# Kernel optimization log

Hardware: AMD Instinct MI355X
Metric: run time of the kernel (lower is better)

Reference implementation:

```python
import jax, jax.numpy as jnp
import numpy as np

D = 1024
H = 16
HD = D // H
DFF = 4 * D
LN_EPS = 1e-5

def layernorm(x, gamma, beta):
    mu = jnp.mean(x, axis=-1, keepdims=True)
    var = jnp.mean(jnp.square(x - mu), axis=-1, keepdims=True)
    return (x - mu) * jax.lax.rsqrt(var + LN_EPS) * gamma + beta

def setup_inputs() -> dict:
    key = jax.random.key(0)
    ks = jax.random.split(key, 10)
    B, Nq, Nk = 2, 2048, 2048
    s = 0.02
    return {
        "q_x": jax.random.normal(ks[0], (B, Nq, D), jnp.float32),
        "kv_x": jax.random.normal(ks[1], (B, Nk, D), jnp.float32),
        "Wq": jax.random.normal(ks[2], (D, D), jnp.float32) * s,
        "Wkv": jax.random.normal(ks[3], (2 * D, D), jnp.float32) * s,
        "Wo": jax.random.normal(ks[4], (D, D), jnp.float32) * s,
        "bo": jnp.zeros((D,), jnp.float32),
        "ln_q_g": jnp.ones((D,), jnp.float32),
        "ln_q_b": jnp.zeros((D,), jnp.float32),
        "ln_kv_g": jnp.ones((D,), jnp.float32),
        "ln_kv_b": jnp.zeros((D,), jnp.float32),
        "W1": jax.random.normal(ks[5], (DFF, D), jnp.float32) * s,
        "b1": jnp.zeros((DFF,), jnp.float32),
        "W2": jax.random.normal(ks[6], (D, DFF), jnp.float32) * s,
        "b2": jnp.zeros((D,), jnp.float32),
    }

def reference(q_x, kv_x, Wq, Wkv, Wo, bo, ln_q_g, ln_q_b, ln_kv_g, ln_kv_b, W1, b1, W2, b2):
    B, Nq, _ = q_x.shape
    Nk = kv_x.shape[1]
    scale = HD ** -0.5
    # norm + projections
    q = layernorm(q_x, ln_q_g, ln_q_b) @ Wq.T                    # [B,Nq,D]
    kv = layernorm(kv_x, ln_kv_g, ln_kv_b) @ Wkv.T               # [B,Nk,2D]
    q = q.reshape(B, Nq, H, HD).transpose(0, 2, 1, 3)            # [B,H,Nq,hd]
    kv = kv.reshape(B, Nk, 2, H, HD).transpose(2, 0, 3, 1, 4)    # [2,B,H,Nk,hd]
    k, v = kv[0], kv[1]
    attn = jnp.einsum('bhqd,bhkd->bhqk', q, k) * scale           # [B,H,Nq,Nk]
    attn = jax.nn.softmax(attn, axis=-1)
    out = jnp.einsum('bhqk,bhkd->bhqd', attn, v)
    out = out.transpose(0, 2, 1, 3).reshape(B, Nq, D)
    x = q_x + out @ Wo.T + bo
    h = jax.nn.silu(x @ W1.T + b1)
    x = x + h @ W2.T + b2
    return x
```

## Files before the change

### kernel.cpp

```cpp
#include <hip/hip_runtime.h>

using u16   = unsigned short;
using f32x4 = __attribute__((ext_vector_type(4))) float;
using s16x8 = __attribute__((ext_vector_type(8))) short;
using u32x2 = __attribute__((ext_vector_type(2))) unsigned int;
using u32x4 = __attribute__((ext_vector_type(4))) unsigned int;

#define LOG2E 1.44269504088896f

static __device__ __forceinline__ u16 f2bf(float f) {
  union { float f; unsigned u; } a; a.f = f;
  unsigned r = a.u + 0x7fffu + ((a.u >> 16) & 1u);
  return (u16)(r >> 16);
}
static __device__ __forceinline__ unsigned cvtpk(float lo, float hi) {
  unsigned r;
  asm("v_cvt_pk_bf16_f32 %0, %1, %2" : "=v"(r) : "v"(lo), "v"(hi));
  return r;
}

static __device__ __forceinline__ void gload16(const void* g, void* l) {
  __builtin_amdgcn_global_load_lds(
      (__attribute__((address_space(1))) unsigned int*)g,
      (__attribute__((address_space(3))) unsigned int*)l, 16, 0, 0);
}

static __device__ __forceinline__ int xcd_swz(int b, int nb) {
  return (b & 7) * (nb >> 3) + (b >> 3);
}

__global__ __launch_bounds__(256) void prep_k(
    const float* __restrict__ Wq, const float* __restrict__ Wkv,
    const float* __restrict__ Wo, const float* __restrict__ W1,
    const float* __restrict__ W2,
    u16* __restrict__ wq_b, u16* __restrict__ wkv_b, u16* __restrict__ wo_b,
    u16* __restrict__ w1_b, u16* __restrict__ w2_b,
    const float* __restrict__ xq, const float* __restrict__ xk,
    const float* __restrict__ gq, const float* __restrict__ bq,
    const float* __restrict__ gk, const float* __restrict__ bk,
    u16* __restrict__ oq, u16* __restrict__ ok)
{
  const int blk = blockIdx.x, t = threadIdx.x;
  if (blk < 12288) {
    const int i = blk * 256 + t;
    const float* src; u16* dst; int off; float sc = 1.0f;
    if      (i <  262144) { src = Wq;  dst = wq_b;  off = i; sc = 0.125f * LOG2E; }
    else if (i <  786432) { src = Wkv; dst = wkv_b; off = i -  262144; }
    else if (i < 1048576) { src = Wo;  dst = wo_b;  off = i -  786432; }
    else if (i < 2097152) { src = W1;  dst = w1_b;  off = i - 1048576; }
    else                  { src = W2;  dst = w2_b;  off = i - 2097152; }
    const float4 v = ((const float4*)src)[off];
    ushort4 o;
    o.x = f2bf(v.x * sc); o.y = f2bf(v.y * sc); o.z = f2bf(v.z * sc); o.w = f2bf(v.w * sc);
    ((ushort4*)dst)[off] = o;
    return;
  }
  int row = blk - 12288;
  const float* x; const float* gam; const float* bet; u16* out;
  if (row < 4096) { x = xq; gam = gq; bet = bq; out = oq; }
  else { row -= 4096; x = xk; gam = gk; bet = bk; out = ok; }
  const float4 v = ((const float4*)(x + (size_t)row * 1024))[t];
  float s  = v.x + v.y + v.z + v.w;
  float ss = v.x*v.x + v.y*v.y + v.z*v.z + v.w*v.w;
  #pragma unroll
  for (int m = 1; m < 64; m <<= 1) { s += __shfl_xor(s, m); ss += __shfl_xor(ss, m); }
  __shared__ float red[8];
  const int w = t >> 6;
  if ((t & 63) == 0) { red[w] = s; red[4 + w] = ss; }
  __syncthreads();
  s  = red[0] + red[1] + red[2] + red[3];
  ss = red[4] + red[5] + red[6] + red[7];
  const float mu   = s * (1.0f / 1024.0f);
  const float rstd = rsqrtf(ss * (1.0f / 1024.0f) - mu * mu + 1e-5f);
  const float4 gv = ((const float4*)gam)[t];
  const float4 bv = ((const float4*)bet)[t];
  ushort4 o;
  o.x = f2bf((v.x - mu) * rstd * gv.x + bv.x);
  o.y = f2bf((v.y - mu) * rstd * gv.y + bv.y);
  o.z = f2bf((v.z - mu) * rstd * gv.z + bv.z);
  o.w = f2bf((v.w - mu) * rstd * gv.w + bv.w);
  ((ushort4*)(out + (size_t)row * 1024))[t] = o;
}

template<int BIAS, int RES, int SILU, int OF32, int OBF>
static __device__ __forceinline__ void gemm_body64(
    const u16* __restrict__ A, const u16* __restrict__ B,
    u16* __restrict__ Cb, float* __restrict__ Cf,
    const float* __restrict__ bias, const float* __restrict__ resid,
    int N, int K, int bid, u16* smem)
{
  const int tid = threadIdx.x;
  const int w = tid >> 6, l = tid & 63;
  const int g = l >> 4, q = l & 15;
  const int ntn = N >> 6;
  const int bm = bid / ntn, bn = bid - bm * ntn;
  const int wr = w >> 1, wc = w & 1;
  const int sw = (q & 7) << 4;
  f32x4 acc[2][2] = {};

  const size_t abase = (size_t)(bm * 128) * K;
  const size_t bbase = (size_t)(bn * 64) * K;

  auto stage = [&](int buf, int k0) {
    u16* as = smem + buf * 8192;
    u16* bs = smem + 16384 + buf * 4096;
    #pragma unroll
    for (int r = 0; r < 2; ++r) {
      const int c = (r << 9) + tid;
      const int row = c >> 3;
      const int sp = (c & 7) ^ (row & 7);
      gload16(A + abase + (size_t)row * K + k0 + sp * 8,
              as + (size_t)((r << 9) + (w << 6)) * 8);
    }
    const int row = tid >> 3;
    const int sp = (tid & 7) ^ (row & 7);
    gload16(B + bbase + (size_t)row * K + k0 + sp * 8,
            bs + (size_t)(w << 6) * 8);
  };

  const int NT = K >> 6;
  stage(0, 0);
  asm volatile("s_waitcnt vmcnt(0)" ::: "memory");
  __syncthreads();
  int cur = 0;
  for (int t = 0; t < NT; ++t) {
    if (t + 1 < NT) stage(cur ^ 1, (t + 1) << 6);
    const char* as = (const char*)(smem + cur * 8192);
    const char* bs = (const char*)(smem + 16384 + cur * 4096);
    #pragma unroll
    for (int ks = 0; ks < 2; ++ks) {
      s16x8 af[2], bfr[2];
      #pragma unroll
      for (int m = 0; m < 2; ++m)
        af[m] = *(const s16x8*)(as + (size_t)(wr * 32 + m * 16 + q) * 128 +
                                ((ks * 64 + g * 16) ^ sw));
      #pragma unroll
      for (int n = 0; n < 2; ++n)
        bfr[n] = *(const s16x8*)(bs + (size_t)(wc * 32 + n * 16 + q) * 128 +
                                 ((ks * 64 + g * 16) ^ sw));
      #pragma unroll
      for (int m = 0; m < 2; ++m)
        #pragma unroll
        for (int n = 0; n < 2; ++n)
          acc[m][n] = __builtin_amdgcn_mfma_f32_16x16x32_bf16(af[m], bfr[n], acc[m][n], 0, 0, 0);
    }
    asm volatile("s_waitcnt vmcnt(0)" ::: "memory");
    __syncthreads();
    cur ^= 1;
  }

  #pragma unroll
  for (int m = 0; m < 2; ++m) {
    const int row0 = bm * 128 + wr * 32 + m * 16 + g * 4;
    #pragma unroll
    for (int n = 0; n < 2; ++n) {
      const int col = bn * 64 + wc * 32 + n * 16 + q;
      float bv = 0.0f;
      if (BIAS) bv = bias[col];
      #pragma unroll
      for (int r = 0; r < 4; ++r) {
        const size_t idx = (size_t)(row0 + r) * N + col;
        float v = acc[m][n][r] + bv;
        if (RES)  v += resid[idx];
        if (SILU) v = v / (1.0f + __expf(-v));
        if (OF32) Cf[idx] = v;
        if (OBF)  Cb[idx] = f2bf(v);
      }
    }
  }
}

template<int BIAS, int RES, int SILU, int OF32, int OBF>
__global__ __launch_bounds__(512, 4) void gemm_k(
    const u16* __restrict__ A, const u16* __restrict__ B,
    u16* __restrict__ Cb, float* __restrict__ Cf,
    const float* __restrict__ bias, const float* __restrict__ resid,
    int N, int K)
{
  __shared__ u16 smem[24576];
  const int bid = xcd_swz(blockIdx.x, gridDim.x);
  gemm_body64<BIAS, RES, SILU, OF32, OBF>(A, B, Cb, Cf, bias, resid, N, K, bid, smem);
}

__global__ __launch_bounds__(512, 4) void gemm_qkv_k(
    const u16* __restrict__ lnq, const u16* __restrict__ wq, u16* __restrict__ qp,
    const u16* __restrict__ lnk, const u16* __restrict__ wkv, u16* __restrict__ kvp)
{
  __shared__ u16 smem[24576];
  const int sbid = xcd_swz(blockIdx.x, 1536);
  if (sbid < 512)
    gemm_body64<0,0,0,0,1>(lnq, wq, qp, nullptr, nullptr, nullptr, 1024, 1024,
                           sbid, smem);
  else
    gemm_body64<0,0,0,0,1>(lnk, wkv, kvp, nullptr, nullptr, nullptr, 2048, 1024,
                           sbid - 512, smem);
}

template<int BIAS, int RES, int SILU, int OF32, int OBF>
__global__ __launch_bounds__(512, 2) void gemm256_k(
    const u16* __restrict__ A, const u16* __restrict__ B,
    u16* __restrict__ Cb, float* __restrict__ Cf,
    const float* __restrict__ bias, const float* __restrict__ resid,
    int N, int K)
{
  __shared__ u16 smem[65536];
  char* smem_c = (char*)smem;
  const int tid = threadIdx.x;
  const int w = tid >> 6, l = tid & 63;
  const int g = l >> 4, q = l & 15;
  const int wm = w >> 2, wn = w & 3;
  const int ntn = N >> 8;
  const int bid = xcd_swz(blockIdx.x, gridDim.x);
  const int bm = bid / ntn, bn = bid - bm * ntn;

  const size_t abase = (size_t)(bm * 256) * K;
  const size_t bbase = (size_t)(bn * 256) * K;

  f32x4 acc[8][4] = {};

  auto stage2 = [&](int buf, int kt, int part) {
    const int isB = part & 1, khalf = part >> 1;
    #pragma unroll
    for (int sub = 0; sub < 2; ++sub) {
      const int row  = sub * 128 + (tid >> 2);
      const int slot = (tid & 3) ^ ((row >> 1) & 3);
      const u16* src = (isB ? B + bbase : A + abase)
                     + (size_t)row * K + kt * 64 + khalf * 32 + slot * 8;
      char* dst = smem_c + buf * 65536 + isB * 32768 + khalf * 16384
                + sub * 8192 + w * 1024;
      gload16(src, dst);
    }
  };

  const int NT = K >> 6;
  stage2(0, 0, 0); stage2(0, 0, 1); stage2(0, 0, 2); stage2(0, 0, 3);
  int cur = 0;
  const int so = (g ^ ((q >> 1) & 3)) * 16;
  for (int t = 0; t < NT; ++t) {
    const bool pre = (t + 1 < NT);
    const char* base = smem_c + cur * 65536;
    #pragma unroll
    for (int ks = 0; ks < 2; ++ks) {
      if (ks == 0 || pre) asm volatile("s_waitcnt vmcnt(4)" ::: "memory");
      else                asm volatile("s_waitcnt vmcnt(0)" ::: "memory");
      asm volatile("" ::: "memory");
      __builtin_amdgcn_s_barrier();
      asm volatile("" ::: "memory");
      const char* Ab = base + ks * 16384;
      const char* Bb = base + 32768 + ks * 16384;
      s16x8 af[8], bf0[2];
      #pragma unroll
      for (int m = 0; m < 8; ++m)
        af[m] = *(const s16x8*)(Ab + (wm * 128 + m * 16 + q) * 64 + so);
      #pragma unroll
      for (int n = 0; n < 2; ++n)
        bf0[n] = *(const s16x8*)(Bb + (wn * 64 + n * 16 + q) * 64 + so);
      if (pre) stage2(cur ^ 1, t + 1, ks * 2);
      asm volatile("s_waitcnt lgkmcnt(0)" ::: "memory");
      __builtin_amdgcn_sched_barrier(0);
      __builtin_amdgcn_s_setprio(1);
      #pragma unroll
      for (int m = 0; m < 8; ++m) {
        acc[m][0] = __builtin_amdgcn_mfma_f32_16x16x32_bf16(af[m], bf0[0], acc[m][0], 0, 0, 0);
        acc[m][1] = __builtin_amdgcn_mfma_f32_16x16x32_bf16(af[m], bf0[1], acc[m][1], 0, 0, 0);
      }
      __builtin_amdgcn_s_setprio(0);
      s16x8 bf1[2];
      #pragma unroll
      for (int n = 0; n < 2; ++n)
        bf1[n] = *(const s16x8*)(Bb + (wn * 64 + (2 + n) * 16 + q) * 64 + so);
      if (pre) stage2(cur ^ 1, t + 1, ks * 2 + 1);
      asm volatile("s_waitcnt lgkmcnt(0)" ::: "memory");
      __builtin_amdgcn_sched_barrier(0);
      __builtin_amdgcn_s_setprio(1);
      #pragma unroll
      for (int m = 0; m < 8; ++m) {
        acc[m][2] = __builtin_amdgcn_mfma_f32_16x16x32_bf16(af[m], bf1[0], acc[m][2], 0, 0, 0);
        acc[m][3] = __builtin_amdgcn_mfma_f32_16x16x32_bf16(af[m], bf1[1], acc[m][3], 0, 0, 0);
      }
      __builtin_amdgcn_s_setprio(0);
    }
    cur ^= 1;
  }

  #pragma unroll
  for (int m = 0; m < 8; ++m) {
    const int row0 = bm * 256 + wm * 128 + m * 16 + g * 4;
    #pragma unroll
    for (int n = 0; n < 4; ++n) {
      const int col = bn * 256 + wn * 64 + n * 16 + q;
      float bv = 0.0f;
      if (BIAS) bv = bias[col];
      #pragma unroll
      for (int r = 0; r < 4; ++r) {
        const size_t idx = (size_t)(row0 + r) * N + col;
        float v = acc[m][n][r] + bv;
        if (RES)  v += resid[idx];
        if (SILU) v = v / (1.0f + __expf(-v));
        if (OF32) Cf[idx] = v;
        if (OBF)  Cb[idx] = f2bf(v);
      }
    }
  }
}

__global__ __launch_bounds__(512, 4) void attn_k(
    const u16* __restrict__ Q, const u16* __restrict__ KV, u16* __restrict__ O)
{
  __shared__ u16 Ks[3][64 * 64];
  __shared__ u16 Vs[3][64 * 64];
  const int tid = threadIdx.x;
  const int w = tid >> 6, l = tid & 63;
  const int g = l >> 4, q = l & 15;
  const int idx = blockIdx.x >> 3;
  const int bh = (blockIdx.x & 7) * 4 + (idx >> 4);
  const int qt = idx & 15;
  const int b = bh >> 4, h = bh & 15;

  const size_t qrow = (size_t)(b * 2048 + qt * 128 + w * 16 + q);
  s16x8 qf[2];
  qf[0] = *(const s16x8*)&Q[qrow * 1024 + h * 64 + g * 8];
  qf[1] = *(const s16x8*)&Q[qrow * 1024 + h * 64 + 32 + g * 8];

  f32x4 oacc[4] = {};
  f32x4 ls = {0.0f, 0.0f, 0.0f, 0.0f};

  const u16* kvb = KV + (size_t)b * 2048 * 2048;
  const unsigned vs_base =
      (unsigned)(unsigned long long)(__attribute__((address_space(3))) u16*)Vs;

  auto stage = [&](int buf, int kv0) {
    const int c = tid;
    const int krow = c >> 3, slot = c & 7;
    gload16(kvb + (size_t)(kv0 + krow) * 2048 + h * 64 + ((slot ^ (krow & 7)) << 3),
            &Ks[buf][(size_t)(w << 6) * 8]);
    const int vkv = ((c >> 3) & 15) * 4 + ((c >> 1) & 3);
    const int vd0 = ((c >> 7) & 3) * 16 + (c & 1) * 8;
    gload16(kvb + (size_t)(kv0 + vkv) * 2048 + 1024 + h * 64 + vd0,
            &Vs[buf][(size_t)(w << 6) * 8]);
  };

  stage(0, 0);
  stage(1, 64);
  int cur = 0;

  for (int kt = 0; kt < 32; ++kt) {
    if (kt < 31) asm volatile("s_waitcnt vmcnt(2)" ::: "memory");
    else         asm volatile("s_waitcnt vmcnt(0)" ::: "memory");
    __builtin_amdgcn_s_barrier();
    asm volatile("" ::: "memory");
    if (kt + 2 < 32) stage((cur == 0) ? 2 : cur - 1, (kt + 2) * 64);

    const char* ksb = (const char*)Ks[cur];
    f32x4 sacc[4] = {};
    __builtin_amdgcn_s_setprio(1);
    #pragma unroll
    for (int s = 0; s < 2; ++s)
      #pragma unroll
      for (int nf = 0; nf < 4; ++nf) {
        const int krw = nf * 16 + q;
        const s16x8 kf = *(const s16x8*)(ksb + krw * 128 +
                              ((s * 64 + g * 16) ^ ((krw & 7) << 4)));
        sacc[nf] = __builtin_amdgcn_mfma_f32_16x16x32_bf16(kf, qf[s], sacc[nf], 0, 0, 0);
      }
    __builtin_amdgcn_s_setprio(0);

    #pragma unroll
    for (int nf = 0; nf < 4; ++nf)
      #pragma unroll
      for (int r = 0; r < 4; ++r)
        sacc[nf][r] = __builtin_amdgcn_exp2f(sacc[nf][r]);
    ls += sacc[0]; ls += sacc[1]; ls += sacc[2]; ls += sacc[3];

    union { u32x4 u; s16x8 s8; } au[2];
    #pragma unroll
    for (int s = 0; s < 2; ++s) {
      au[s].u[0] = cvtpk(sacc[2*s  ][0], sacc[2*s  ][1]);
      au[s].u[1] = cvtpk(sacc[2*s  ][2], sacc[2*s  ][3]);
      au[s].u[2] = cvtpk(sacc[2*s+1][0], sacc[2*s+1][1]);
      au[s].u[3] = cvtpk(sacc[2*s+1][2], sacc[2*s+1][3]);
    }

    const unsigned a0 = vs_base + (unsigned)(cur * 8192) + (unsigned)(g * 128 + 2 * q);
    u32x2 v0,v1,v2,v3,v4,v5,v6,v7,v8,v9,v10,v11,v12,v13,v14,v15;
    asm volatile(
        "ds_read_b64_tr_b16 %0,  %16\n\t"
        "ds_read_b64_tr_b16 %1,  %16 offset:512\n\t"
        "ds_read_b64_tr_b16 %2,  %16 offset:2048\n\t"
        "ds_read_b64_tr_b16 %3,  %16 offset:2560\n\t"
        "ds_read_b64_tr_b16 %4,  %16 offset:4096\n\t"
        "ds_read_b64_tr_b16 %5,  %16 offset:4608\n\t"
        "ds_read_b64_tr_b16 %6,  %16 offset:6144\n\t"
        "ds_read_b64_tr_b16 %7,  %16 offset:6656\n\t"
        "ds_read_b64_tr_b16 %8,  %16 offset:1024\n\t"
        "ds_read_b64_tr_b16 %9,  %16 offset:1536\n\t"
        "ds_read_b64_tr_b16 %10, %16 offset:3072\n\t"
        "ds_read_b64_tr_b16 %11, %16 offset:3584\n\t"
        "ds_read_b64_tr_b16 %12, %16 offset:5120\n\t"
        "ds_read_b64_tr_b16 %13, %16 offset:5632\n\t"
        "ds_read_b64_tr_b16 %14, %16 offset:7168\n\t"
        "ds_read_b64_tr_b16 %15, %16 offset:7680\n\t"
        "s_waitcnt lgkmcnt(0)"
        : "=&v"(v0), "=&v"(v1), "=&v"(v2),  "=&v"(v3),
          "=&v"(v4), "=&v"(v5), "=&v"(v6),  "=&v"(v7),
          "=&v"(v8), "=&v"(v9), "=&v"(v10), "=&v"(v11),
          "=&v"(v12),"=&v"(v13),"=&v"(v14), "=&v"(v15)
        : "v"(a0) : "memory");
    __builtin_amdgcn_sched_barrier(0);

    __builtin_amdgcn_s_setprio(1);
    {
      union { u32x4 u; s16x8 s8; } bu;
      bu.u[0]=v0[0];  bu.u[1]=v0[1];  bu.u[2]=v1[0];  bu.u[3]=v1[1];
      oacc[0] = __builtin_amdgcn_mfma_f32_16x16x32_bf16(au[0].s8, bu.s8, oacc[0], 0, 0, 0);
      bu.u[0]=v2[0];  bu.u[1]=v2[1];  bu.u[2]=v3[0];  bu.u[3]=v3[1];
      oacc[1] = __builtin_amdgcn_mfma_f32_16x16x32_bf16(au[0].s8, bu.s8, oacc[1], 0, 0, 0);
      bu.u[0]=v4[0];  bu.u[1]=v4[1];  bu.u[2]=v5[0];  bu.u[3]=v5[1];
      oacc[2] = __builtin_amdgcn_mfma_f32_16x16x32_bf16(au[0].s8, bu.s8, oacc[2], 0, 0, 0);
      bu.u[0]=v6[0];  bu.u[1]=v6[1];  bu.u[2]=v7[0];  bu.u[3]=v7[1];
      oacc[3] = __builtin_amdgcn_mfma_f32_16x16x32_bf16(au[0].s8, bu.s8, oacc[3], 0, 0, 0);
      bu.u[0]=v8[0];  bu.u[1]=v8[1];  bu.u[2]=v9[0];  bu.u[3]=v9[1];
      oacc[0] = __builtin_amdgcn_mfma_f32_16x16x32_bf16(au[1].s8, bu.s8, oacc[0], 0, 0, 0);
      bu.u[0]=v10[0]; bu.u[1]=v10[1]; bu.u[2]=v11[0]; bu.u[3]=v11[1];
      oacc[1] = __builtin_amdgcn_mfma_f32_16x16x32_bf16(au[1].s8, bu.s8, oacc[1], 0, 0, 0);
      bu.u[0]=v12[0]; bu.u[1]=v12[1]; bu.u[2]=v13[0]; bu.u[3]=v13[1];
      oacc[2] = __builtin_amdgcn_mfma_f32_16x16x32_bf16(au[1].s8, bu.s8, oacc[2], 0, 0, 0);
      bu.u[0]=v14[0]; bu.u[1]=v14[1]; bu.u[2]=v15[0]; bu.u[3]=v15[1];
      oacc[3] = __builtin_amdgcn_mfma_f32_16x16x32_bf16(au[1].s8, bu.s8, oacc[3], 0, 0, 0);
    }
    __builtin_amdgcn_s_setprio(0);

    cur = (cur == 2) ? 0 : cur + 1;
  }

  float lsum = (ls[0] + ls[1]) + (ls[2] + ls[3]);
  lsum += __shfl_xor(lsum, 16);
  lsum += __shfl_xor(lsum, 32);
  float lr[4];
  #pragma unroll
  for (int r = 0; r < 4; ++r) lr[r] = __shfl(lsum, g * 4 + r);
  const size_t ob = (size_t)(b * 2048 + qt * 128 + w * 16) * 1024 + h * 64;
  #pragma unroll
  for (int r = 0; r < 4; ++r) {
    const float inv = 1.0f / lr[r];
    #pragma unroll
    for (int nf = 0; nf < 4; ++nf)
      O[ob + (size_t)(g * 4 + r) * 1024 + nf * 16 + q] = f2bf(oacc[nf][r] * inv);
  }
}

extern "C" void kernel_launch(void* const* d_in, const int* in_sizes, int n_in,
                              void* d_out, int out_size, void* d_ws, size_t ws_size,
                              hipStream_t stream)
{
  const float* q_x  = (const float*)d_in[0];
  const float* kv_x = (const float*)d_in[1];
  const float* Wq   = (const float*)d_in[2];
  const float* Wkv  = (const float*)d_in[3];
  const float* Wo   = (const float*)d_in[4];
  const float* bo   = (const float*)d_in[5];
  const float* lnqg = (const float*)d_in[6];
  const float* lnqb = (const float*)d_in[7];
  const float* lnkg = (const float*)d_in[8];
  const float* lnkb = (const float*)d_in[9];
  const float* W1   = (const float*)d_in[10];
  const float* b1   = (const float*)d_in[11];
  const float* W2   = (const float*)d_in[12];
  const float* b2   = (const float*)d_in[13];
  float* out = (float*)d_out;

  char* ws = (char*)d_ws;
  const size_t MB = 1024 * 1024;
  u16*   wq_b  = (u16*)  (ws +  0 * MB);
  u16*   wkv_b = (u16*)  (ws +  2 * MB);
  u16*   wo_b  = (u16*)  (ws +  6 * MB);
  u16*   w1_b  = (u16*)  (ws +  8 * MB);
  u16*   w2_b  = (u16*)  (ws + 16 * MB);
  u16*   lnq   = (u16*)  (ws + 24 * MB);
  u16*   lnk   = (u16*)  (ws + 32 * MB);
  u16*   qp    = (u16*)  (ws + 40 * MB);
  u16*   kvp   = (u16*)  (ws + 48 * MB);
  u16*   ao    = (u16*)  (ws + 64 * MB);
  float* xf    = (float*)(ws + 72 * MB);
  u16*   xb    = (u16*)  (ws + 88 * MB);
  u16*   hb    = (u16*)  (ws + 96 * MB);

  prep_k<<<dim3(20480), dim3(256), 0, stream>>>(
      Wq, Wkv, Wo, W1, W2, wq_b, wkv_b, wo_b, w1_b, w2_b,
      q_x, kv_x, lnqg, lnqb, lnkg, lnkb, lnq, lnk);

  gemm_qkv_k<<<dim3(1536), dim3(512), 0, stream>>>(lnq, wq_b, qp, lnk, wkv_b, kvp);
  attn_k<<<dim3(512), dim3(512), 0, stream>>>(qp, kvp, ao);
  gemm_k<1,1,0,1,1><<<dim3(512),  dim3(512), 0, stream>>>(
      ao, wo_b, xb, xf, bo, q_x, 1024, 1024);
  gemm256_k<1,0,1,0,1><<<dim3(256), dim3(512), 0, stream>>>(
      xb, w1_b, hb, nullptr, b1, nullptr, 4096, 1024);
  gemm_k<1,1,0,1,0><<<dim3(512),  dim3(512), 0, stream>>>(
      hb, w2_b, nullptr, out, b2, xf, 1024, 4096);
}
```

Before: 195.1 us.

## Split-K the W2 GEMM with a reduction kernel; use 128x64 tiles for W1

The FFN down-projection (K=4096) is split into two K-halves computed by 1024 blocks that write fp32 partials. A separate elementwise kernel then sums the partials with the residual and bias. The W1 GEMM drops the 256x256 tile kernel in favour of the 128x64 tile kernel with 2048 blocks. The aim is more parallelism and shorter per-block K loops, at the cost of extra fp32 partial traffic, an extra launch, and less data reuse per tile in W1.

```diff
diff --git a/kernel.cpp b/kernel.cpp
--- a/kernel.cpp
+++ b/kernel.cpp
@@ -83,11 +83,11 @@
 }
 
 template<int BIAS, int RES, int SILU, int OF32, int OBF>
-static __device__ __forceinline__ void gemm_body64(
+static __device__ __forceinline__ void gemm_body64_2buf(
     const u16* __restrict__ A, const u16* __restrict__ B,
     u16* __restrict__ Cb, float* __restrict__ Cf,
     const float* __restrict__ bias, const float* __restrict__ resid,
-    int N, int K, int bid, u16* smem)
+    int N, int Kst, int Klen, int bid, u16* smem)
 {
   const int tid = threadIdx.x;
   const int w = tid >> 6, l = tid & 63;
@@ -98,8 +98,8 @@
   const int sw = (q & 7) << 4;
   f32x4 acc[2][2] = {};
 
-  const size_t abase = (size_t)(bm * 128) * K;
-  const size_t bbase = (size_t)(bn * 64) * K;
+  const size_t abase = (size_t)(bm * 128) * Kst;
+  const size_t bbase = (size_t)(bn * 64) * Kst;
 
   auto stage = [&](int buf, int k0) {
     u16* as = smem + buf * 8192;
@@ -109,16 +109,16 @@
       const int c = (r << 9) + tid;
       const int row = c >> 3;
       const int sp = (c & 7) ^ (row & 7);
-      gload16(A + abase + (size_t)row * K + k0 + sp * 8,
+      gload16(A + abase + (size_t)row * Kst + k0 + sp * 8,
               as + (size_t)((r << 9) + (w << 6)) * 8);
     }
     const int row = tid >> 3;
     const int sp = (tid & 7) ^ (row & 7);
-    gload16(B + bbase + (size_t)row * K + k0 + sp * 8,
+    gload16(B + bbase + (size_t)row * Kst + k0 + sp * 8,
             bs + (size_t)(w << 6) * 8);
   };
 
-  const int NT = K >> 6;
+  const int NT = Klen >> 6;
   stage(0, 0);
   asm volatile("s_waitcnt vmcnt(0)" ::: "memory");
   __syncthreads();
@@ -171,7 +171,7 @@
 }
 
 template<int BIAS, int RES, int SILU, int OF32, int OBF>
-__global__ __launch_bounds__(512, 4) void gemm_k(
+__global__ __launch_bounds__(512, 4) void gemm_k2(
     const u16* __restrict__ A, const u16* __restrict__ B,
     u16* __restrict__ Cb, float* __restrict__ Cf,
     const float* __restrict__ bias, const float* __restrict__ resid,
@@ -179,7 +179,8 @@
 {
   __shared__ u16 smem[24576];
   const int bid = xcd_swz(blockIdx.x, gridDim.x);
-  gemm_body64<BIAS, RES, SILU, OF32, OBF>(A, B, Cb, Cf, bias, resid, N, K, bid, smem);
+  gemm_body64_2buf<BIAS, RES, SILU, OF32, OBF>(A, B, Cb, Cf, bias, resid,
+                                               N, K, K, bid, smem);
 }
 
 __global__ __launch_bounds__(512, 4) void gemm_qkv_k(
@@ -189,119 +190,42 @@
   __shared__ u16 smem[24576];
   const int sbid = xcd_swz(blockIdx.x, 1536);
   if (sbid < 512)
-    gemm_body64<0,0,0,0,1>(lnq, wq, qp, nullptr, nullptr, nullptr, 1024, 1024,
-                           sbid, smem);
+    gemm_body64_2buf<0,0,0,0,1>(lnq, wq, qp, nullptr, nullptr, nullptr,
+                                1024, 1024, 1024, sbid, smem);
   else
-    gemm_body64<0,0,0,0,1>(lnk, wkv, kvp, nullptr, nullptr, nullptr, 2048, 1024,
-                           sbid - 512, smem);
-}
-
-template<int BIAS, int RES, int SILU, int OF32, int OBF>
-__global__ __launch_bounds__(512, 2) void gemm256_k(
+    gemm_body64_2buf<0,0,0,0,1>(lnk, wkv, kvp, nullptr, nullptr, nullptr,
+                                2048, 1024, 1024, sbid - 512, smem);
+}
+
+__global__ __launch_bounds__(512, 4) void gemm_w2sk_k(
     const u16* __restrict__ A, const u16* __restrict__ B,
-    u16* __restrict__ Cb, float* __restrict__ Cf,
-    const float* __restrict__ bias, const float* __restrict__ resid,
-    int N, int K)
-{
-  __shared__ u16 smem[65536];
-  char* smem_c = (char*)smem;
-  const int tid = threadIdx.x;
-  const int w = tid >> 6, l = tid & 63;
-  const int g = l >> 4, q = l & 15;
-  const int wm = w >> 2, wn = w & 3;
-  const int ntn = N >> 8;
-  const int bid = xcd_swz(blockIdx.x, gridDim.x);
-  const int bm = bid / ntn, bn = bid - bm * ntn;
-
-  const size_t abase = (size_t)(bm * 256) * K;
-  const size_t bbase = (size_t)(bn * 256) * K;
-
-  f32x4 acc[8][4] = {};
-
-  auto stage2 = [&](int buf, int kt, int part) {
-    const int isB = part & 1, khalf = part >> 1;
-    #pragma unroll
-    for (int sub = 0; sub < 2; ++sub) {
-      const int row  = sub * 128 + (tid >> 2);
-      const int slot = (tid & 3) ^ ((row >> 1) & 3);
-      const u16* src = (isB ? B + bbase : A + abase)
-                     + (size_t)row * K + kt * 64 + khalf * 32 + slot * 8;
-      char* dst = smem_c + buf * 65536 + isB * 32768 + khalf * 16384
-                + sub * 8192 + w * 1024;
-      gload16(src, dst);
-    }
-  };
-
-  const int NT = K >> 6;
-  stage2(0, 0, 0); stage2(0, 0, 1); stage2(0, 0, 2); stage2(0, 0, 3);
-  int cur = 0;
-  const int so = (g ^ ((q >> 1) & 3)) * 16;
-  for (int t = 0; t < NT; ++t) {
-    const bool pre = (t + 1 < NT);
-    const char* base = smem_c + cur * 65536;
-    #pragma unroll
-    for (int ks = 0; ks < 2; ++ks) {
-      if (ks == 0 || pre) asm volatile("s_waitcnt vmcnt(4)" ::: "memory");
-      else                asm volatile("s_waitcnt vmcnt(0)" ::: "memory");
-      asm volatile("" ::: "memory");
-      __builtin_amdgcn_s_barrier();
-      asm volatile("" ::: "memory");
-      const char* Ab = base + ks * 16384;
-      const char* Bb = base + 32768 + ks * 16384;
-      s16x8 af[8], bf0[2];
-      #pragma unroll
-      for (int m = 0; m < 8; ++m)
-        af[m] = *(const s16x8*)(Ab + (wm * 128 + m * 16 + q) * 64 + so);
-      #pragma unroll
-      for (int n = 0; n < 2; ++n)
-        bf0[n] = *(const s16x8*)(Bb + (wn * 64 + n * 16 + q) * 64 + so);
-      if (pre) stage2(cur ^ 1, t + 1, ks * 2);
-      asm volatile("s_waitcnt lgkmcnt(0)" ::: "memory");
-      __builtin_amdgcn_sched_barrier(0);
-      __builtin_amdgcn_s_setprio(1);
-      #pragma unroll
-      for (int m = 0; m < 8; ++m) {
-        acc[m][0] = __builtin_amdgcn_mfma_f32_16x16x32_bf16(af[m], bf0[0], acc[m][0], 0, 0, 0);
-        acc[m][1] = __builtin_amdgcn_mfma_f32_16x16x32_bf16(af[m], bf0[1], acc[m][1], 0, 0, 0);
-      }
-      __builtin_amdgcn_s_setprio(0);
-      s16x8 bf1[2];
-      #pragma unroll
-      for (int n = 0; n < 2; ++n)
-        bf1[n] = *(const s16x8*)(Bb + (wn * 64 + (2 + n) * 16 + q) * 64 + so);
-      if (pre) stage2(cur ^ 1, t + 1, ks * 2 + 1);
-      asm volatile("s_waitcnt lgkmcnt(0)" ::: "memory");
-      __builtin_amdgcn_sched_barrier(0);
-      __builtin_amdgcn_s_setprio(1);
-      #pragma unroll
-      for (int m = 0; m < 8; ++m) {
-        acc[m][2] = __builtin_amdgcn_mfma_f32_16x16x32_bf16(af[m], bf1[0], acc[m][2], 0, 0, 0);
-        acc[m][3] = __builtin_amdgcn_mfma_f32_16x16x32_bf16(af[m], bf1[1], acc[m][3], 0, 0, 0);
-      }
-      __builtin_amdgcn_s_setprio(0);
-    }
-    cur ^= 1;
-  }
-
-  #pragma unroll
-  for (int m = 0; m < 8; ++m) {
-    const int row0 = bm * 256 + wm * 128 + m * 16 + g * 4;
-    #pragma unroll
-    for (int n = 0; n < 4; ++n) {
-      const int col = bn * 256 + wn * 64 + n * 16 + q;
-      float bv = 0.0f;
-      if (BIAS) bv = bias[col];
-      #pragma unroll
-      for (int r = 0; r < 4; ++r) {
-        const size_t idx = (size_t)(row0 + r) * N + col;
-        float v = acc[m][n][r] + bv;
-        if (RES)  v += resid[idx];
-        if (SILU) v = v / (1.0f + __expf(-v));
-        if (OF32) Cf[idx] = v;
-        if (OBF)  Cb[idx] = f2bf(v);
-      }
-    }
-  }
+    float* __restrict__ p0, float* __restrict__ p1)
+{
+  __shared__ u16 smem[24576];
+  const int sb = xcd_swz(blockIdx.x, 1024);
+  const int kc = sb >> 9;
+  const int tb = sb & 511;
+  gemm_body64_2buf<0,0,0,1,0>(A + kc * 2048, B + kc * 2048,
+                              nullptr, kc ? p1 : p0, nullptr, nullptr,
+                              1024, 4096, 2048, tb, smem);
+}
+
+__global__ __launch_bounds__(256) void red_k(
+    const float* __restrict__ p0, const float* __restrict__ p1,
+    const float* __restrict__ xf, const float* __restrict__ b2,
+    float* __restrict__ out)
+{
+  const int i = blockIdx.x * 256 + threadIdx.x;
+  const float4 a = ((const float4*)p0)[i];
+  const float4 b = ((const float4*)p1)[i];
+  const float4 c = ((const float4*)xf)[i];
+  const float4 d = ((const float4*)b2)[i & 255];
+  float4 o;
+  o.x = a.x + b.x + c.x + d.x;
+  o.y = a.y + b.y + c.y + d.y;
+  o.z = a.z + b.z + c.z + d.z;
+  o.w = a.w + b.w + c.w + d.w;
+  ((float4*)out)[i] = o;
 }
 
 __global__ __launch_bounds__(512, 4) void attn_k(
@@ -484,6 +408,8 @@
   float* xf    = (float*)(ws + 72 * MB);
   u16*   xb    = (u16*)  (ws + 88 * MB);
   u16*   hb    = (u16*)  (ws + 96 * MB);
+  float* p0    = (float*)(ws + 24 * MB);
+  float* p1    = (float*)(ws + 40 * MB);
 
   prep_k<<<dim3(20480), dim3(256), 0, stream>>>(
       Wq, Wkv, Wo, W1, W2, wq_b, wkv_b, wo_b, w1_b, w2_b,
@@ -491,10 +417,10 @@
 
   gemm_qkv_k<<<dim3(1536), dim3(512), 0, stream>>>(lnq, wq_b, qp, lnk, wkv_b, kvp);
   attn_k<<<dim3(512), dim3(512), 0, stream>>>(qp, kvp, ao);
-  gemm_k<1,1,0,1,1><<<dim3(512),  dim3(512), 0, stream>>>(
+  gemm_k2<1,1,0,1,1><<<dim3(512),  dim3(512), 0, stream>>>(
       ao, wo_b, xb, xf, bo, q_x, 1024, 1024);
-  gemm256_k<1,0,1,0,1><<<dim3(256), dim3(512), 0, stream>>>(
+  gemm_k2<1,0,1,0,1><<<dim3(2048), dim3(512), 0, stream>>>(
       xb, w1_b, hb, nullptr, b1, nullptr, 4096, 1024);
-  gemm_k<1,1,0,1,0><<<dim3(512),  dim3(512), 0, stream>>>(
-      hb, w2_b, nullptr, out, b2, xf, 1024, 4096);
-}
+  gemm_w2sk_k<<<dim3(1024), dim3(512), 0, stream>>>(hb, w2_b, p0, p1);
+  red_k<<<dim3(4096), dim3(256), 0, stream>>>(p0, p1, xf, b2, out);
+}
```

Measured after the change: 220.7 us. +13.1%, slower.
